# Kernel optimization log

Measured on AMD Instinct MI355X. Metric: run time of the kernel, lower is better.

## Reference

```python
import jax, jax.numpy as jnp
import numpy as np
from jax import lax

NH, K, V, TOPK = 8, 64, 64, 4  # n_heads, key_size, val_size, SparseAttention top_k(=3+1)
EPS = 1e-7
BN_EPS = 1e-5


def conv1x1(x, w, b):
    # x: [B,C,H,W], w: [O,C] -> [B,O,H,W]
    return jnp.einsum('oc,bchw->bohw', w, x) + b[None, :, None, None]


def conv3x3(x, w, b):
    y = lax.conv_general_dilated(x, w, (1, 1), 'SAME',
                                 dimension_numbers=('NCHW', 'OIHW', 'NCHW'))
    return y + b[None, :, None, None]


def batchnorm(x, g, b):
    # training-mode BN over (N,H,W), biased variance (matches torch BatchNorm2d in train)
    m = jnp.mean(x, axis=(0, 2, 3), keepdims=True)
    v = jnp.var(x, axis=(0, 2, 3), keepdims=True)
    return (x - m) * lax.rsqrt(v + BN_EPS) * g[None, :, None, None] + b[None, :, None, None]


def to_flat(y, d):
    # [B, NH*d, H, W] -> [B*H*W*NH, d]
    B, _, H, W = y.shape
    return y.reshape(B, NH, d, H, W).transpose(0, 3, 4, 1, 2).reshape(B * H * W * NH, d)


def setup_inputs() -> dict:
    key = jax.random.key(0)
    ks = jax.random.split(key, 16)
    L, C, B, H, W = 4, 256, 8, 32, 32
    KH, VH = K * NH, V * NH
    s = 0.02
    return {
        'x': jax.random.normal(ks[0], (B, C, H, W), jnp.float32),
        'kw': jax.random.normal(ks[1], (L, KH, C), jnp.float32) * s,
        'kb': jax.random.normal(ks[2], (L, KH), jnp.float32) * s,
        'qw': jax.random.normal(ks[3], (L, KH, C), jnp.float32) * s,
        'qb': jax.random.normal(ks[4], (L, KH), jnp.float32) * s,
        'vw': jax.random.normal(ks[5], (L, VH, C), jnp.float32) * s,
        'vb': jax.random.normal(ks[6], (L, VH), jnp.float32) * s,
        'ow1': jax.random.normal(ks[7], (L, C, VH, 3, 3), jnp.float32) * s,
        'ob1': jax.random.normal(ks[8], (L, C), jnp.float32) * s,
        'bn_g': jnp.ones((L, C), jnp.float32),
        'bn_b': jnp.zeros((L, C), jnp.float32),
        'ow2': jax.random.normal(ks[9], (L, C, C, 3, 3), jnp.float32) * s,
        'ob2': jax.random.normal(ks[10], (L, C), jnp.float32) * s,
        'gammas': jax.random.normal(ks[11], (L,), jnp.float32),
    }


def reference(x, kw, kb, qw, qb, vw, vb, ow1, ob1, bn_g, bn_b, ow2, ob2, gammas):
    B, C, H, W = x.shape
    L = kw.shape[0]
    temp = jnp.asarray(np.power(K, 0.5), x.dtype)  # concentration=0.5
    keys, vals = [], []
    for l in range(L):  # structurally distinct layers: growing key/val list
        keys.append(to_flat(conv1x1(x, kw[l], kb[l]), K))  # [N,K]
        vals.append(to_flat(conv1x1(x, vw[l], vb[l]), V))  # [N,V]
        q = to_flat(conv1x1(x, qw[l], qb[l]), K)           # [N,K]
        kt = jnp.stack(keys + [jnp.zeros_like(keys[0])], axis=1)  # [N,T,K] zero key appended
        vt = jnp.stack(vals + [jnp.zeros_like(vals[0])], axis=1)  # [N,T,V]
        scores = jnp.einsum('nk,ntk->nt', q / temp, kt)
        attn = jax.nn.softmax(scores, axis=-1)
        T = attn.shape[1]
        if T > TOPK:  # SparseAttention: topk threshold, clamp, renormalize
            delta = lax.top_k(attn, TOPK)[0][:, -1] + EPS
            wgt = jnp.maximum(attn - delta[:, None], 0.0)
            attn = wgt / (jnp.sum(wgt, axis=1, keepdims=True) + EPS)
        o = jnp.einsum('nt,ntv->nv', attn, vt)  # [N,V]
        o = o.reshape(B, H, W, NH * V).transpose(0, 3, 1, 2)  # [B, NH*V, H, W]
        h1 = jax.nn.relu(batchnorm(conv3x3(o, ow1[l], ob1[l]), bn_g[l], bn_b[l]))
        h2 = conv3x3(h1, ow2[l], ob2[l])
        x = x + h2 * gammas[l]
    return x
```

## Files before the change

### kernel.cpp

```cpp
#include <hip/hip_runtime.h>


typedef __attribute__((ext_vector_type(8))) short short8;
typedef __attribute__((ext_vector_type(4))) float f32x4;
typedef __attribute__((ext_vector_type(2))) float f32x2;
typedef __attribute__((ext_vector_type(4))) unsigned short ushort4_t;
typedef __attribute__((ext_vector_type(4))) unsigned int uint4_t;

#define NTOK 65536
#define NPIX 8192

__device__ __forceinline__ float bf2f(unsigned short u) {
  unsigned int v = ((unsigned int)u) << 16;
  float f; __builtin_memcpy(&f, &v, 4); return f;
}
__device__ __forceinline__ unsigned short f2bf(float f) {
  unsigned int u; __builtin_memcpy(&u, &f, 4);
  u = (u + 0x7FFFu + ((u >> 16) & 1u)) >> 16;
  return (unsigned short)u;
}
__device__ __forceinline__ float blo(unsigned int u) {
  unsigned int v = u << 16; float f; __builtin_memcpy(&f, &v, 4); return f;
}
__device__ __forceinline__ float bhi(unsigned int u) {
  unsigned int v = u & 0xFFFF0000u; float f; __builtin_memcpy(&f, &v, 4); return f;
}

__device__ __forceinline__ void gl_lds16(const unsigned short* g, const unsigned short* l) {
  __builtin_amdgcn_global_load_lds(
      (const __attribute__((address_space(1))) unsigned int*)g,
      (__attribute__((address_space(3))) unsigned int*)l, 16, 0, 0);
}

__global__ void k_prep(const float* __restrict__ kw, const float* __restrict__ vw,
                       const float* __restrict__ qw, const float* __restrict__ ow1,
                       const float* __restrict__ ow2, const float* __restrict__ kb,
                       const float* __restrict__ vb, const float* __restrict__ qb,
                       unsigned short* __restrict__ wkqv, unsigned short* __restrict__ w1,
                       unsigned short* __restrict__ w2, float* __restrict__ biascat,
                       unsigned int* __restrict__ opad_u32, unsigned int* __restrict__ h1pad_u32) {
  long i = (long)blockIdx.x * 256 + threadIdx.x;
  if (i < 1572864) {
    int idx = (int)(i & 131071); int sl = (int)(i >> 17); int slot = sl % 3, l = sl / 3;
    const float* s = slot == 0 ? kw : slot == 1 ? vw : qw;
    wkqv[i] = f2bf(s[(size_t)l * 131072 + idx]);
    return;
  }
  i -= 1572864;
  if (i < 4718592) {
    int c = (int)(i % 512), tap = (int)((i / 512) % 9); long m = i / 4608;
    w1[i] = f2bf(ow1[(m * 512 + c) * 9 + tap]);
    return;
  }
  i -= 4718592;
  if (i < 2359296) {
    int c = (int)(i % 256), tap = (int)((i / 256) % 9); long m = i / 2304;
    w2[i] = f2bf(ow2[(m * 256 + c) * 9 + tap]);
    return;
  }
  i -= 2359296;
  if (i < 6144) {
    int o = (int)(i & 511); int sl = (int)(i >> 9); int slot = sl % 3, l = sl / 3;
    const float* s = slot == 0 ? kb : slot == 1 ? vb : qb;
    biascat[i] = s[l * 512 + o];
    return;
  }
  i -= 6144;
  auto border_pix = [](int pidx) -> size_t {
    const int b = pidx / 132, t = pidx % 132;
    int y, x;
    if (t < 34) { y = 0; x = t; }
    else if (t < 68) { y = 33; x = t - 34; }
    else { const int j = t - 68; y = 1 + (j >> 1); x = (j & 1) * 33; }
    return (size_t)b * 1156 + y * 34 + x;
  };
  if (i < 270336) {
    const int pidx = (int)(i >> 8), c = (int)(i & 255);
    opad_u32[border_pix(pidx) * 256 + c] = 0u;
    return;
  }
  i -= 270336;
  if (i < 135168) {
    const int pidx = (int)(i >> 7), c = (int)(i & 127);
    h1pad_u32[border_pix(pidx) * 128 + c] = 0u;
  }
}

__global__ __launch_bounds__(256) void k_x2cl(const float* __restrict__ src,
                                              float* __restrict__ xacc,
                                              unsigned short* __restrict__ dst) {
  __shared__ unsigned short t[64][68];
  const int hw0 = blockIdx.x * 64, b = blockIdx.y;
  const int tid = threadIdx.x;
  for (int cc = 0; cc < 4; cc++) {
    __syncthreads();
    {
      const int px = tid & 63, c = tid >> 6;
      #pragma unroll
      for (int i = 0; i < 16; i++) {
        const size_t idx = ((size_t)b * 256 + cc * 64 + c + i * 4) * 1024 + hw0 + px;
        const float v = src[idx];
        xacc[idx] = v;
        t[px][c + i * 4] = f2bf(v);
      }
    }
    __syncthreads();
    {
      const int px = tid >> 2, c0 = (tid & 3) * 16;
      unsigned short* dp = dst + ((size_t)b * 1024 + hw0 + px) * 256 + cc * 64 + c0;
      short8 v0, v1;
      #pragma unroll
      for (int i = 0; i < 8; i++) { v0[i] = (short)t[px][c0 + i]; v1[i] = (short)t[px][c0 + 8 + i]; }
      *(short8*)dp = v0; *(short8*)(dp + 8) = v1;
    }
  }
}

template<int MODE, int NSTEP, int KDIM, int CIN, int NBUF>
__global__ __launch_bounds__(256) void k_gemm(
    const unsigned short* __restrict__ W,
    const unsigned short* __restrict__ act,
    const float* __restrict__ bias,
    int l,
    unsigned short* __restrict__ ktok, unsigned short* __restrict__ vtok,
    unsigned short* __restrict__ qtok,
    unsigned short* __restrict__ pout) {
  __shared__ unsigned short sm[NBUF][2][8192];

  const int bid = blockIdx.x;
  int m0, b, pix0, s;
  if constexpr (MODE == 0) {
    const int xcd = bid & 7, li = bid >> 3;
    const int nt = xcd * 8 + (li & 7);
    m0 = (li >> 3) * 128; s = 0;
    b = nt >> 3; pix0 = (nt & 7) * 128;
  } else {
    const int xcd = bid & 7, li = bid >> 3;
    const int nt = xcd * 8 + (li & 7);
    const int r = li >> 3;
    m0 = (r & 1) * 128; s = r >> 1;
    b = nt >> 3; pix0 = (nt & 7) * 128;
  }
  constexpr int SW = (MODE == 1) ? 128 : 64;

  const int tid = threadIdx.x;
  const int wid = tid >> 6, lane = tid & 63;
  const int lr = lane & 15, lg = lane >> 4;
  const int m_off = (wid >> 1) * 64, n_off = (wid & 1) * 64;

  const unsigned short* gA[4];
  const unsigned short* gB[4];
  #pragma unroll
  for (int j = 0; j < 4; j++) {
    const int o = (wid * 4 + j) * 512 + lane * 8;
    const int row = o >> 6;
    const int ksw = (((o >> 3) & 7) ^ (row & 7)) * 8;
    gA[j] = W + (size_t)(m0 + row) * KDIM + (MODE ? s * SW : 0) + ksw;
    if constexpr (MODE == 0) {
      gB[j] = act + ((size_t)b * 1024 + pix0 + row) * 256 + ksw;
    } else {
      const int pix = pix0 + row, py = pix >> 5, px = pix & 31;
      gB[j] = act + (size_t)b * 1156 * CIN + ((size_t)py * 34 + px) * CIN + s * SW + ksw;
    }
  }

  auto offA = [&](int st) -> int {
    if constexpr (MODE == 0) return st * 64;
    else if constexpr (MODE == 1) return (st >> 1) * 512 + (st & 1) * 64;
    else return st * 256;
  };
  auto offB = [&](int st) -> int {
    if constexpr (MODE == 0) return st * 64;
    else if constexpr (MODE == 1) {
      const int tap = st >> 1, dy = tap / 3, dx = tap - dy * 3;
      return (dy * 34 + dx) * 512 + (st & 1) * 64;
    } else {
      const int dy = st / 3, dx = st - dy * 3;
      return (dy * 34 + dx) * 256;
    }
  };
  auto STAGE = [&](int bf, int st) {
    const int oa = offA(st), ob = offB(st);
    #pragma unroll
    for (int j = 0; j < 4; j++) gl_lds16(gA[j] + oa, &sm[bf][0][(wid * 4 + j) * 512]);
    #pragma unroll
    for (int j = 0; j < 4; j++) gl_lds16(gB[j] + ob, &sm[bf][1][(wid * 4 + j) * 512]);
  };
  auto COMPUTE = [&](int cur, f32x4 (*acc)[4]) {
    #pragma unroll
    for (int ks = 0; ks < 2; ks++) {
      short8 af[4], bfr[4];
      #pragma unroll
      for (int i = 0; i < 4; i++) {
        const int ra = m_off + i * 16 + lr;
        af[i] = *(const short8*)&sm[cur][0][ra * 64 + (((ks * 4 + lg) ^ (ra & 7)) * 8)];
        const int rb = n_off + i * 16 + lr;
        bfr[i] = *(const short8*)&sm[cur][1][rb * 64 + (((ks * 4 + lg) ^ (rb & 7)) * 8)];
      }
      #pragma unroll
      for (int i = 0; i < 4; i++)
        #pragma unroll
        for (int jn = 0; jn < 4; jn++)
          acc[i][jn] = __builtin_amdgcn_mfma_f32_16x16x32_bf16(af[i], bfr[jn], acc[i][jn], 0, 0, 0);
    }
  };

  f32x4 acc[4][4] = {};

  if constexpr (NBUF == 2) {
    STAGE(0, 0);
    __syncthreads();
    #pragma unroll
    for (int st = 0; st < NSTEP; st++) {
      if (st + 1 < NSTEP) STAGE((st + 1) & 1, st + 1);
      COMPUTE(st & 1, acc);
      __syncthreads();
    }
  } else {
    #pragma unroll
    for (int st = 0; st < NSTEP; st++) {
      if (st) __syncthreads();
      STAGE(0, st);
      __syncthreads();
      COMPUTE(0, acc);
    }
  }

  if constexpr (MODE == 0) {
    #pragma unroll
    for (int mi = 0; mi < 4; mi++) {
      const int mb = m0 + m_off + mi * 16 + lg * 4;
      const int tensor = mb >> 9, head = (mb >> 6) & 7, d0 = mb & 63;
      unsigned short* dst = (tensor == 0) ? ktok + (size_t)l * NTOK * 64
                          : (tensor == 1) ? vtok + (size_t)l * NTOK * 64 : qtok;
      const float b0 = bias[mb], b1 = bias[mb + 1], b2 = bias[mb + 2], b3 = bias[mb + 3];
      #pragma unroll
      for (int ni = 0; ni < 4; ni++) {
        const int n = pix0 + n_off + ni * 16 + lr;
        ushort4_t pk;
        pk[0] = f2bf(acc[mi][ni][0] + b0); pk[1] = f2bf(acc[mi][ni][1] + b1);
        pk[2] = f2bf(acc[mi][ni][2] + b2); pk[3] = f2bf(acc[mi][ni][3] + b3);
        *(ushort4_t*)&dst[(((size_t)b * 1024 + n) * 8 + head) * 64 + d0] = pk;
      }
    }
  } else {
    #pragma unroll
    for (int mi = 0; mi < 4; mi++) {
      const int mb = m0 + m_off + mi * 16 + lg * 4;
      unsigned short* orow = pout + (size_t)(s * 256 + mb) * 8192 + (size_t)b * 1024 + pix0;
      #pragma unroll
      for (int ni = 0; ni < 4; ni++) {
        const int n = n_off + ni * 16 + lr;
        #pragma unroll
        for (int r = 0; r < 4; r++) orow[(size_t)r * 8192 + n] = f2bf(acc[mi][ni][r]);
      }
    }
  }
}

template<int L>
__global__ __launch_bounds__(256) void k_attn(const unsigned int* __restrict__ q_tok,
                                              const unsigned int* __restrict__ k_tok,
                                              const unsigned int* __restrict__ v_tok,
                                              unsigned int* __restrict__ opad) {
  constexpr int T = L + 2;
  const int lane = threadIdx.x & 63, wid = threadIdx.x >> 6;
  const int ti = lane >> 2, dq = lane & 3;
  const int token = blockIdx.x * 64 + wid * 16 + ti;
  const size_t rowq = (size_t)token * 32 + dq * 8;

  unsigned int q[8];
  *(uint4_t*)&q[0] = *(const uint4_t*)(q_tok + rowq);
  *(uint4_t*)&q[4] = *(const uint4_t*)(q_tok + rowq + 4);
  float qf[16];
  #pragma unroll
  for (int j = 0; j < 8; j++) {
    qf[2 * j]     = blo(q[j]) * 0.125f;
    qf[2 * j + 1] = bhi(q[j]) * 0.125f;
  }

  float s[T];
  s[T - 1] = 0.0f;
  #pragma unroll
  for (int t = 0; t <= L; t++) {
    const unsigned int* kp = k_tok + (size_t)t * (NTOK * 32) + rowq;
    unsigned int kk[8];
    *(uint4_t*)&kk[0] = *(const uint4_t*)kp;
    *(uint4_t*)&kk[4] = *(const uint4_t*)(kp + 4);
    float p = 0.0f;
    #pragma unroll
    for (int j = 0; j < 8; j++) {
      p = fmaf(qf[2 * j], blo(kk[j]), p);
      p = fmaf(qf[2 * j + 1], bhi(kk[j]), p);
    }
    p += __shfl_xor(p, 1);
    p += __shfl_xor(p, 2);
    s[t] = p;
  }

  float mx = s[0];
  #pragma unroll
  for (int t = 1; t < T; t++) mx = fmaxf(mx, s[t]);
  float attn[T], sum = 0.0f;
  #pragma unroll
  for (int t = 0; t < T; t++) { attn[t] = __expf(s[t] - mx); sum += attn[t]; }
  const float inv = 1.0f / sum;
  #pragma unroll
  for (int t = 0; t < T; t++) attn[t] *= inv;

  if constexpr (T == 5) {
    float m1 = attn[0], m2 = 1e30f;
    #pragma unroll
    for (int t = 1; t < 5; t++) {
      const float a = attn[t];
      const float nm1 = fminf(m1, a);
      m2 = fminf(m2, fmaxf(m1, a));
      m1 = nm1;
    }
    const float delta = m2 + 1e-7f;
    float ws = 0.0f;
    #pragma unroll
    for (int t = 0; t < 5; t++) { attn[t] = fmaxf(attn[t] - delta, 0.0f); ws += attn[t]; }
    const float r = 1.0f / (ws + 1e-7f);
    #pragma unroll
    for (int t = 0; t < 5; t++) attn[t] *= r;
  }

  float o[16];
  #pragma unroll
  for (int i = 0; i < 16; i++) o[i] = 0.0f;
  #pragma unroll
  for (int t = 0; t <= L; t++) {
    const unsigned int* vp = v_tok + (size_t)t * (NTOK * 32) + rowq;
    unsigned int vv[8];
    *(uint4_t*)&vv[0] = *(const uint4_t*)vp;
    *(uint4_t*)&vv[4] = *(const uint4_t*)(vp + 4);
    const float a = attn[t];
    #pragma unroll
    for (int j = 0; j < 8; j++) {
      o[2 * j]     = fmaf(a, blo(vv[j]), o[2 * j]);
      o[2 * j + 1] = fmaf(a, bhi(vv[j]), o[2 * j + 1]);
    }
  }

  unsigned int po[8];
  #pragma unroll
  for (int j = 0; j < 8; j++) {
    unsigned int r;
    asm("v_cvt_pk_bf16_f32 %0, %1, %2" : "=v"(r) : "v"(o[2 * j]), "v"(o[2 * j + 1]));
    po[j] = r;
  }
  const int head = token & 7, pix = token >> 3;
  const int b = pix >> 10, hw = pix & 1023, y = hw >> 5, x = hw & 31;
  unsigned int* dp = opad +
      (((size_t)b * 1156 + (y + 1) * 34 + (x + 1)) * 512 + head * 64 + dq * 16) / 2;
  *(uint4_t*)dp = *(uint4_t*)&po[0];
  *(uint4_t*)(dp + 4) = *(uint4_t*)&po[4];
}

__global__ __launch_bounds__(512) void k_comb_stats(const unsigned int* __restrict__ p,
    const float* __restrict__ bias1, const float* __restrict__ g, const float* __restrict__ bta,
    unsigned int* __restrict__ h1c, float* __restrict__ stats) {
  const int c = blockIdx.x, tid = threadIdx.x;
  const float bs = bias1[c];
  const unsigned int* P0 = p + (size_t)c * 4096;
  unsigned int* H = h1c + (size_t)c * 4096;
  float s = 0.0f, ss = 0.0f;
  #pragma unroll
  for (int k2 = 0; k2 < 2; k2++) {
    const int j = (k2 * 512 + tid) * 4;
    uint4_t a0 = *(const uint4_t*)(P0 + j);
    uint4_t a1 = *(const uint4_t*)(P0 + 1048576 + j);
    uint4_t a2 = *(const uint4_t*)(P0 + 2097152 + j);
    uint4_t a3 = *(const uint4_t*)(P0 + 3145728 + j);
    uint4_t o;
    #pragma unroll
    for (int e = 0; e < 4; e++) {
      const float vl = blo(a0[e]) + blo(a1[e]) + blo(a2[e]) + blo(a3[e]) + bs;
      const float vh = bhi(a0[e]) + bhi(a1[e]) + bhi(a2[e]) + bhi(a3[e]) + bs;
      s += vl + vh; ss += vl * vl + vh * vh;
      o[e] = (unsigned int)f2bf(vl) | ((unsigned int)f2bf(vh) << 16);
    }
    *(uint4_t*)(H + j) = o;
  }
  #pragma unroll
  for (int o2 = 32; o2 > 0; o2 >>= 1) { s += __shfl_xor(s, o2); ss += __shfl_xor(ss, o2); }
  __shared__ float rs[8], rss[8];
  const int wid = tid >> 6, lane = tid & 63;
  if (lane == 0) { rs[wid] = s; rss[wid] = ss; }
  __syncthreads();
  if (tid == 0) {
    float S = 0.0f, SS = 0.0f;
    #pragma unroll
    for (int w = 0; w < 8; w++) { S += rs[w]; SS += rss[w]; }
    const float m = S * (1.0f / 8192.0f);
    const float var = SS * (1.0f / 8192.0f) - m * m;
    const float A = g[c] * rsqrtf(var + 1e-5f);
    stats[c] = A;
    stats[256 + c] = bta[c] - m * A;
  }
}

__global__ __launch_bounds__(512) void k_bn_relu_pad(const unsigned int* __restrict__ h1c,
    const float* __restrict__ stats, unsigned short* __restrict__ hpad) {
  __shared__ unsigned short t[32][264];
  const int hw0 = blockIdx.x * 32, b = blockIdx.y, tid = threadIdx.x;
  const int u = tid & 15, cg = tid >> 4;
  const int base = ((b * 1024 + hw0) >> 1);
  #pragma unroll
  for (int i = 0; i < 8; i++) {
    const int ch = i * 32 + cg;
    const float A = stats[ch], Bt = stats[256 + ch];
    const unsigned int a = h1c[(size_t)ch * 4096 + base + u];
    t[2 * u][ch]     = f2bf(fmaxf(blo(a) * A + Bt, 0.0f));
    t[2 * u + 1][ch] = f2bf(fmaxf(bhi(a) * A + Bt, 0.0f));
  }
  __syncthreads();
  const int px = tid >> 4, c0 = (tid & 15) * 16;
  const int y = hw0 >> 5, x = hw0 & 31;
  unsigned short* dp = hpad + ((size_t)b * 1156 + (y + 1) * 34 + (x + px + 1)) * 256 + c0;
  short8 v0, v1;
  #pragma unroll
  for (int i = 0; i < 8; i++) { v0[i] = (short)t[px][c0 + i]; v1[i] = (short)t[px][c0 + 8 + i]; }
  *(short8*)dp = v0; *(short8*)(dp + 8) = v1;
}

__global__ __launch_bounds__(512) void k_comb2(const unsigned int* __restrict__ p,
    const float* __restrict__ bias2, const float* __restrict__ gamma_p, int last,
    float* __restrict__ xacc, unsigned short* __restrict__ xcl) {
  __shared__ unsigned short t[32][264];
  const int hw0 = blockIdx.x * 32, b = blockIdx.y, tid = threadIdx.x;
  const int u = tid & 15, cg = tid >> 4;
  const float gmm = gamma_p[0];
  const int base = ((b * 1024 + hw0) >> 1);
  #pragma unroll
  for (int i = 0; i < 8; i++) {
    const int ch = i * 32 + cg;
    const float bs = bias2[ch];
    const size_t j = (size_t)ch * 4096 + base + u;
    const unsigned int a0 = p[j];
    const unsigned int a1 = p[j + 1048576];
    const unsigned int a2 = p[j + 2097152];
    const unsigned int a3 = p[j + 3145728];
    const float vl = blo(a0) + blo(a1) + blo(a2) + blo(a3) + bs;
    const float vh = bhi(a0) + bhi(a1) + bhi(a2) + bhi(a3) + bs;
    float* X = xacc + ((size_t)b * 256 + ch) * 1024 + hw0 + 2 * u;
    f32x2 xv = *(const f32x2*)X;
    const float xl = xv[0] + gmm * vl;
    const float xh = xv[1] + gmm * vh;
    f32x2 xw = {xl, xh};
    *(f32x2*)X = xw;
    t[2 * u][ch]     = f2bf(xl);
    t[2 * u + 1][ch] = f2bf(xh);
  }
  __syncthreads();
  if (!last) {
    const int px = tid >> 4, c0 = (tid & 15) * 16;
    unsigned short* dp = xcl + ((size_t)b * 1024 + hw0 + px) * 256 + c0;
    short8 v0, v1;
    #pragma unroll
    for (int i = 0; i < 8; i++) { v0[i] = (short)t[px][c0 + i]; v1[i] = (short)t[px][c0 + 8 + i]; }
    *(short8*)dp = v0; *(short8*)(dp + 8) = v1;
  }
}

extern "C" void kernel_launch(void* const* d_in, const int* in_sizes, int n_in,
                              void* d_out, int out_size, void* d_ws, size_t ws_size,
                              hipStream_t stream) {
  (void)in_sizes; (void)n_in; (void)out_size;
  const float* x_in   = (const float*)d_in[0];
  const float* kw     = (const float*)d_in[1];
  const float* kb     = (const float*)d_in[2];
  const float* qw     = (const float*)d_in[3];
  const float* qb     = (const float*)d_in[4];
  const float* vw     = (const float*)d_in[5];
  const float* vb     = (const float*)d_in[6];
  const float* ow1    = (const float*)d_in[7];
  const float* ob1    = (const float*)d_in[8];
  const float* bn_g   = (const float*)d_in[9];
  const float* bn_b   = (const float*)d_in[10];
  const float* ow2    = (const float*)d_in[11];
  const float* ob2    = (const float*)d_in[12];
  const float* gammas = (const float*)d_in[13];

  char* ws = (char*)d_ws;
  size_t off = 0;
  auto alloc = [&](size_t bytes) -> void* {
    void* pp = ws + off;
    off += (bytes + 255) & ~(size_t)255;
    return pp;
  };
  unsigned short* xcl     = (unsigned short*)alloc((size_t)NPIX * 256 * 2);
  unsigned short* k_tok   = (unsigned short*)alloc((size_t)4 * NTOK * 64 * 2);
  unsigned short* v_tok   = (unsigned short*)alloc((size_t)4 * NTOK * 64 * 2);
  unsigned short* q_tok   = (unsigned short*)alloc((size_t)NTOK * 64 * 2);
  unsigned short* opad    = (unsigned short*)alloc((size_t)8 * 1156 * 512 * 2);
  unsigned int*   h1c     = (unsigned int*)alloc((size_t)256 * 4096 * 4);
  unsigned short* h1pad   = (unsigned short*)alloc((size_t)8 * 1156 * 256 * 2);
  unsigned short* p1      = (unsigned short*)alloc((size_t)4 * 256 * 8192 * 2);
  float*          stats   = (float*)alloc(512 * 4);
  unsigned short* wkqv    = (unsigned short*)alloc((size_t)4 * 3 * 512 * 256 * 2);
  unsigned short* w1bf    = (unsigned short*)alloc((size_t)1024 * 4608 * 2);
  unsigned short* w2bf    = (unsigned short*)alloc((size_t)1024 * 2304 * 2);
  float*          biascat = (float*)alloc((size_t)6144 * 4);
  if (off > ws_size) return;

  float* xacc = (float*)d_out;

  k_prep<<<35400, 256, 0, stream>>>(kw, vw, qw, ow1, ow2, kb, vb, qb,
                                    wkqv, w1bf, w2bf, biascat,
                                    (unsigned int*)opad, (unsigned int*)h1pad);
  k_x2cl<<<dim3(16, 8), 256, 0, stream>>>(x_in, xacc, xcl);

  for (int l = 0; l < 4; l++) {
    k_gemm<0, 4, 256, 256, 1><<<768, 256, 0, stream>>>(
        wkqv + (size_t)l * 3 * 512 * 256, xcl, biascat + l * 1536, l,
        k_tok, v_tok, q_tok, nullptr);
    const unsigned int* qt = (const unsigned int*)q_tok;
    const unsigned int* kt = (const unsigned int*)k_tok;
    const unsigned int* vt = (const unsigned int*)v_tok;
    unsigned int* op = (unsigned int*)opad;
    switch (l) {
      case 0: k_attn<0><<<1024, 256, 0, stream>>>(qt, kt, vt, op); break;
      case 1: k_attn<1><<<1024, 256, 0, stream>>>(qt, kt, vt, op); break;
      case 2: k_attn<2><<<1024, 256, 0, stream>>>(qt, kt, vt, op); break;
      default: k_attn<3><<<1024, 256, 0, stream>>>(qt, kt, vt, op); break;
    }
    k_gemm<1, 18, 4608, 512, 2><<<512, 256, 0, stream>>>(
        w1bf + (size_t)l * 256 * 4608, opad, nullptr, l,
        nullptr, nullptr, nullptr, p1);
    k_comb_stats<<<256, 512, 0, stream>>>((const unsigned int*)p1, ob1 + l * 256,
                                          bn_g + l * 256, bn_b + l * 256, h1c, stats);
    k_bn_relu_pad<<<dim3(32, 8), 512, 0, stream>>>(h1c, stats, h1pad);
    k_gemm<2, 9, 2304, 256, 2><<<512, 256, 0, stream>>>(
        w2bf + (size_t)l * 256 * 2304, h1pad, nullptr, l,
        nullptr, nullptr, nullptr, p1);
    k_comb2<<<dim3(32, 8), 512, 0, stream>>>((const unsigned int*)p1, ob2 + l * 256,
                                             gammas + l, (l == 3) ? 1 : 0, xacc, xcl);
  }
}
```

Measured before the change: 353.1 us.

## Fuse x layout conversion into prep, fold q scale into weights, drop h1c buffer

Merges the x-to-channels-last conversion into the prep kernel as extra blocks, which saves one launch. It folds the 1/sqrt(K) query scale into the q weights and bias so the attention kernel skips a multiply per element. The conv weight reorder now reads the source coalesced and scatters the writes. The bf16 h1c intermediate is removed: BN-relu-pad now re-reads and re-sums the four split-K partials, trading an extra write/read of h1c for re-reading four partial buffers.

```diff
diff --git a/kernel.cpp b/kernel.cpp
--- a/kernel.cpp
+++ b/kernel.cpp
@@ -9,6 +9,7 @@
 
 #define NTOK 65536
 #define NPIX 8192
+#define PREP_FLAT_BLOCKS 35400
 
 __device__ __forceinline__ float bf2f(unsigned short u) {
   unsigned int v = ((unsigned int)u) << 16;
@@ -38,31 +39,69 @@
                        const float* __restrict__ vb, const float* __restrict__ qb,
                        unsigned short* __restrict__ wkqv, unsigned short* __restrict__ w1,
                        unsigned short* __restrict__ w2, float* __restrict__ biascat,
-                       unsigned int* __restrict__ opad_u32, unsigned int* __restrict__ h1pad_u32) {
+                       unsigned int* __restrict__ opad_u32, unsigned int* __restrict__ h1pad_u32,
+                       const float* __restrict__ x_in, float* __restrict__ xacc,
+                       unsigned short* __restrict__ xcl) {
+  if (blockIdx.x >= PREP_FLAT_BLOCKS) {
+    __shared__ unsigned short t[64][68];
+    const int xb = blockIdx.x - PREP_FLAT_BLOCKS;
+    const int hw0 = (xb & 15) * 64, b = xb >> 4;
+    const int tid = threadIdx.x;
+    for (int cc = 0; cc < 4; cc++) {
+      __syncthreads();
+      {
+        const int px = tid & 63, c = tid >> 6;
+        #pragma unroll
+        for (int i = 0; i < 16; i++) {
+          const size_t idx = ((size_t)b * 256 + cc * 64 + c + i * 4) * 1024 + hw0 + px;
+          const float v = x_in[idx];
+          xacc[idx] = v;
+          t[px][c + i * 4] = f2bf(v);
+        }
+      }
+      __syncthreads();
+      {
+        const int px = tid >> 2, c0 = (tid & 3) * 16;
+        unsigned short* dp = xcl + ((size_t)b * 1024 + hw0 + px) * 256 + cc * 64 + c0;
+        short8 v0, v1;
+        #pragma unroll
+        for (int i = 0; i < 8; i++) { v0[i] = (short)t[px][c0 + i]; v1[i] = (short)t[px][c0 + 8 + i]; }
+        *(short8*)dp = v0; *(short8*)(dp + 8) = v1;
+      }
+    }
+    return;
+  }
+
   long i = (long)blockIdx.x * 256 + threadIdx.x;
   if (i < 1572864) {
     int idx = (int)(i & 131071); int sl = (int)(i >> 17); int slot = sl % 3, l = sl / 3;
     const float* s = slot == 0 ? kw : slot == 1 ? vw : qw;
-    wkqv[i] = f2bf(s[(size_t)l * 131072 + idx]);
+    float v = s[(size_t)l * 131072 + idx];
+    if (slot == 2) v *= 0.125f;
+    wkqv[i] = f2bf(v);
     return;
   }
   i -= 1572864;
   if (i < 4718592) {
-    int c = (int)(i % 512), tap = (int)((i / 512) % 9); long m = i / 4608;
-    w1[i] = f2bf(ow1[(m * 512 + c) * 9 + tap]);
+    long m = i / 4608; int r = (int)(i % 4608);
+    int c = r / 9, tap = r - 9 * c;
+    w1[m * 4608 + tap * 512 + c] = f2bf(ow1[i]);
     return;
   }
   i -= 4718592;
   if (i < 2359296) {
-    int c = (int)(i % 256), tap = (int)((i / 256) % 9); long m = i / 2304;
-    w2[i] = f2bf(ow2[(m * 256 + c) * 9 + tap]);
+    long m = i / 2304; int r = (int)(i % 2304);
+    int c = r / 9, tap = r - 9 * c;
+    w2[m * 2304 + tap * 256 + c] = f2bf(ow2[i]);
     return;
   }
   i -= 2359296;
   if (i < 6144) {
     int o = (int)(i & 511); int sl = (int)(i >> 9); int slot = sl % 3, l = sl / 3;
     const float* s = slot == 0 ? kb : slot == 1 ? vb : qb;
-    biascat[i] = s[l * 512 + o];
+    float v = s[l * 512 + o];
+    if (slot == 2) v *= 0.125f;
+    biascat[i] = v;
     return;
   }
   i -= 6144;
@@ -83,36 +122,6 @@
   if (i < 135168) {
     const int pidx = (int)(i >> 7), c = (int)(i & 127);
     h1pad_u32[border_pix(pidx) * 128 + c] = 0u;
-  }
-}
-
-__global__ __launch_bounds__(256) void k_x2cl(const float* __restrict__ src,
-                                              float* __restrict__ xacc,
-                                              unsigned short* __restrict__ dst) {
-  __shared__ unsigned short t[64][68];
-  const int hw0 = blockIdx.x * 64, b = blockIdx.y;
-  const int tid = threadIdx.x;
-  for (int cc = 0; cc < 4; cc++) {
-    __syncthreads();
-    {
-      const int px = tid & 63, c = tid >> 6;
-      #pragma unroll
-      for (int i = 0; i < 16; i++) {
-        const size_t idx = ((size_t)b * 256 + cc * 64 + c + i * 4) * 1024 + hw0 + px;
-        const float v = src[idx];
-        xacc[idx] = v;
-        t[px][c + i * 4] = f2bf(v);
-      }
-    }
-    __syncthreads();
-    {
-      const int px = tid >> 2, c0 = (tid & 3) * 16;
-      unsigned short* dp = dst + ((size_t)b * 1024 + hw0 + px) * 256 + cc * 64 + c0;
-      short8 v0, v1;
-      #pragma unroll
-      for (int i = 0; i < 8; i++) { v0[i] = (short)t[px][c0 + i]; v1[i] = (short)t[px][c0 + 8 + i]; }
-      *(short8*)dp = v0; *(short8*)(dp + 8) = v1;
-    }
   }
 }
 
@@ -275,8 +284,8 @@
   float qf[16];
   #pragma unroll
   for (int j = 0; j < 8; j++) {
-    qf[2 * j]     = blo(q[j]) * 0.125f;
-    qf[2 * j + 1] = bhi(q[j]) * 0.125f;
+    qf[2 * j]     = blo(q[j]);
+    qf[2 * j + 1] = bhi(q[j]);
   }
 
   float s[T];
@@ -360,11 +369,10 @@
 
 __global__ __launch_bounds__(512) void k_comb_stats(const unsigned int* __restrict__ p,
     const float* __restrict__ bias1, const float* __restrict__ g, const float* __restrict__ bta,
-    unsigned int* __restrict__ h1c, float* __restrict__ stats) {
+    float* __restrict__ stats) {
   const int c = blockIdx.x, tid = threadIdx.x;
   const float bs = bias1[c];
   const unsigned int* P0 = p + (size_t)c * 4096;
-  unsigned int* H = h1c + (size_t)c * 4096;
   float s = 0.0f, ss = 0.0f;
   #pragma unroll
   for (int k2 = 0; k2 < 2; k2++) {
@@ -373,15 +381,12 @@
     uint4_t a1 = *(const uint4_t*)(P0 + 1048576 + j);
     uint4_t a2 = *(const uint4_t*)(P0 + 2097152 + j);
     uint4_t a3 = *(const uint4_t*)(P0 + 3145728 + j);
-    uint4_t o;
     #pragma unroll
     for (int e = 0; e < 4; e++) {
       const float vl = blo(a0[e]) + blo(a1[e]) + blo(a2[e]) + blo(a3[e]) + bs;
       const float vh = bhi(a0[e]) + bhi(a1[e]) + bhi(a2[e]) + bhi(a3[e]) + bs;
       s += vl + vh; ss += vl * vl + vh * vh;
-      o[e] = (unsigned int)f2bf(vl) | ((unsigned int)f2bf(vh) << 16);
-    }
-    *(uint4_t*)(H + j) = o;
+    }
   }
   #pragma unroll
   for (int o2 = 32; o2 > 0; o2 >>= 1) { s += __shfl_xor(s, o2); ss += __shfl_xor(ss, o2); }
@@ -401,8 +406,9 @@
   }
 }
 
-__global__ __launch_bounds__(512) void k_bn_relu_pad(const unsigned int* __restrict__ h1c,
-    const float* __restrict__ stats, unsigned short* __restrict__ hpad) {
+__global__ __launch_bounds__(512) void k_bn_relu_pad(const unsigned int* __restrict__ p,
+    const float* __restrict__ bias1, const float* __restrict__ stats,
+    unsigned short* __restrict__ hpad) {
   __shared__ unsigned short t[32][264];
   const int hw0 = blockIdx.x * 32, b = blockIdx.y, tid = threadIdx.x;
   const int u = tid & 15, cg = tid >> 4;
@@ -410,10 +416,17 @@
   #pragma unroll
   for (int i = 0; i < 8; i++) {
     const int ch = i * 32 + cg;
+    const float bs = bias1[ch];
     const float A = stats[ch], Bt = stats[256 + ch];
-    const unsigned int a = h1c[(size_t)ch * 4096 + base + u];
-    t[2 * u][ch]     = f2bf(fmaxf(blo(a) * A + Bt, 0.0f));
-    t[2 * u + 1][ch] = f2bf(fmaxf(bhi(a) * A + Bt, 0.0f));
+    const size_t j = (size_t)ch * 4096 + base + u;
+    const unsigned int a0 = p[j];
+    const unsigned int a1 = p[j + 1048576];
+    const unsigned int a2 = p[j + 2097152];
+    const unsigned int a3 = p[j + 3145728];
+    const float vl = blo(a0) + blo(a1) + blo(a2) + blo(a3) + bs;
+    const float vh = bhi(a0) + bhi(a1) + bhi(a2) + bhi(a3) + bs;
+    t[2 * u][ch]     = f2bf(fmaxf(vl * A + Bt, 0.0f));
+    t[2 * u + 1][ch] = f2bf(fmaxf(vh * A + Bt, 0.0f));
   }
   __syncthreads();
   const int px = tid >> 4, c0 = (tid & 15) * 16;
@@ -495,7 +508,6 @@
   unsigned short* v_tok   = (unsigned short*)alloc((size_t)4 * NTOK * 64 * 2);
   unsigned short* q_tok   = (unsigned short*)alloc((size_t)NTOK * 64 * 2);
   unsigned short* opad    = (unsigned short*)alloc((size_t)8 * 1156 * 512 * 2);
-  unsigned int*   h1c     = (unsigned int*)alloc((size_t)256 * 4096 * 4);
   unsigned short* h1pad   = (unsigned short*)alloc((size_t)8 * 1156 * 256 * 2);
   unsigned short* p1      = (unsigned short*)alloc((size_t)4 * 256 * 8192 * 2);
   float*          stats   = (float*)alloc(512 * 4);
@@ -507,10 +519,11 @@
 
   float* xacc = (float*)d_out;
 
-  k_prep<<<35400, 256, 0, stream>>>(kw, vw, qw, ow1, ow2, kb, vb, qb,
-                                    wkqv, w1bf, w2bf, biascat,
-                                    (unsigned int*)opad, (unsigned int*)h1pad);
-  k_x2cl<<<dim3(16, 8), 256, 0, stream>>>(x_in, xacc, xcl);
+  k_prep<<<PREP_FLAT_BLOCKS + 128, 256, 0, stream>>>(
+      kw, vw, qw, ow1, ow2, kb, vb, qb,
+      wkqv, w1bf, w2bf, biascat,
+      (unsigned int*)opad, (unsigned int*)h1pad,
+      x_in, xacc, xcl);
 
   for (int l = 0; l < 4; l++) {
     k_gemm<0, 4, 256, 256, 1><<<768, 256, 0, stream>>>(
@@ -530,8 +543,9 @@
         w1bf + (size_t)l * 256 * 4608, opad, nullptr, l,
         nullptr, nullptr, nullptr, p1);
     k_comb_stats<<<256, 512, 0, stream>>>((const unsigned int*)p1, ob1 + l * 256,
-                                          bn_g + l * 256, bn_b + l * 256, h1c, stats);
-    k_bn_relu_pad<<<dim3(32, 8), 512, 0, stream>>>(h1c, stats, h1pad);
+                                          bn_g + l * 256, bn_b + l * 256, stats);
+    k_bn_relu_pad<<<dim3(32, 8), 512, 0, stream>>>((const unsigned int*)p1,
+                                                   ob1 + l * 256, stats, h1pad);
     k_gemm<2, 9, 2304, 256, 2><<<512, 256, 0, stream>>>(
         w2bf + (size_t)l * 256 * 2304, h1pad, nullptr, l,
         nullptr, nullptr, nullptr, p1);
```

New measurement: 357.2 us. Within noise of the previous version (+1.2%).
